# Kernel tuning notes

Hardware: AMD Instinct MI355X
Metric: run time of the kernel (lower is better)

## Reference

```python
import jax, jax.numpy as jnp
import numpy as np

NEG = -9e15  # mask value from original (-9000000000000000.0)

def setup_inputs() -> dict:
    key = jax.random.key(0)
    k1, k2, k3, k4 = jax.random.split(key, 4)
    N, nin, nout = 8192, 256, 128
    h = jax.random.normal(k1, (N, nin), dtype=jnp.float32)
    adj = jax.random.randint(k2, (N, N), 0, 2, dtype=jnp.int32)
    w = jax.random.normal(k3, (nin, nout), dtype=jnp.float32)
    v = jax.random.normal(k4, (2 * nout, 1), dtype=jnp.float32)
    return {"h": h, "adj": adj, "w": w, "v": v}

def reference(h, adj, w, v):
    nout = w.shape[1]
    hw = h @ w                      # [N, nout]
    hw1 = hw @ v[:nout]             # [N, 1]
    hw2 = hw @ v[nout:]             # [N, 1]
    eij = hw1 + hw2.T               # [N, N] additive outer-sum scores
    att = jnp.where(adj > 0, eij, jnp.float32(NEG))
    att = jax.nn.softmax(att, axis=1)
    return att @ hw                 # [N, nout]
```

## Files before the change

### kernel.cpp

```cpp
#include <hip/hip_runtime.h>
#include <math.h>

#define N_ROWS 8192
#define NIN    256
#define NOUT   128
#define CUTOFF 45.0f
#define TOPK   32
#define NBINS  256
#define RANGE  384.0f
#define MAXL   256

__device__ __forceinline__ float block_max_256(float v, float* red) {
#pragma unroll
    for (int off = 32; off > 0; off >>= 1)
        v = fmaxf(v, __shfl_down(v, off, 64));
    if ((threadIdx.x & 63) == 0) red[threadIdx.x >> 6] = v;
    __syncthreads();
    float r = fmaxf(fmaxf(red[0], red[1]), fmaxf(red[2], red[3]));
    __syncthreads();
    return r;
}

__global__ __launch_bounds__(256) void k_sw(const float* __restrict__ h,
                                            const float* __restrict__ w,
                                            const float* __restrict__ v,
                                            float* __restrict__ s) {
    __shared__ float wv[NIN];
    int tid = threadIdx.x;
    const float* wr = w + (size_t)tid * NOUT;
    const float* v2 = v + NOUT;
    float acc = 0.f;
#pragma unroll
    for (int n = 0; n < NOUT; n += 4) {
        float4 a = *(const float4*)(wr + n);
        float4 b = *(const float4*)(v2 + n);
        acc = fmaf(a.x, b.x, acc);
        acc = fmaf(a.y, b.y, acc);
        acc = fmaf(a.z, b.z, acc);
        acc = fmaf(a.w, b.w, acc);
    }
    wv[tid] = acc;
    __syncthreads();

    int wid  = tid >> 6;
    int lane = tid & 63;
    float4 wv4 = *(const float4*)(wv + lane * 4);
    int row0 = blockIdx.x * 8 + wid * 2;
#pragma unroll
    for (int r = 0; r < 2; ++r) {
        const float* hr = h + (size_t)(row0 + r) * NIN;
        float4 hv = *(const float4*)(hr + lane * 4);
        float a = hv.x * wv4.x;
        a = fmaf(hv.y, wv4.y, a);
        a = fmaf(hv.z, wv4.z, a);
        a = fmaf(hv.w, wv4.w, a);
#pragma unroll
        for (int off = 32; off > 0; off >>= 1)
            a += __shfl_down(a, off, 64);
        if (lane == 0) s[row0 + r] = a;
    }
}

__global__ __launch_bounds__(256) void k_top(const float* __restrict__ s_g,
                                             int* __restrict__ L,
                                             float* __restrict__ Ls,
                                             int* __restrict__ nL_p,
                                             float* __restrict__ T_p) {
    __shared__ float sd[N_ROWS];
    __shared__ float red[4];
    __shared__ int   hist[NBINS];
    __shared__ int   c;
    __shared__ float Tsh;
    int tid = threadIdx.x;
    hist[tid] = 0;
    float mloc = -INFINITY;
    for (int j = tid; j < N_ROWS; j += 256) {
        float v = s_g[j];
        sd[j] = v;
        mloc = fmaxf(mloc, v);
    }
    __syncthreads();
    float mstar = block_max_256(mloc, red);
    const float invw = (float)NBINS / RANGE;
    for (int j = tid; j < N_ROWS; j += 256) {
        int b = (int)((mstar - sd[j]) * invw);
        b = b < 0 ? 0 : (b > NBINS - 1 ? NBINS - 1 : b);
        atomicAdd(&hist[b], 1);
    }
    __syncthreads();
    if (tid == 0) {
        int cum = 0, B = NBINS - 1;
        for (int b = 0; b < NBINS; ++b) {
            cum += hist[b];
            if (cum >= TOPK) { B = b; break; }
        }
        Tsh = mstar - (float)(B + 1) * (RANGE / (float)NBINS) - CUTOFF;
        *T_p = Tsh;
        c = 0;
    }
    __syncthreads();
    float T = Tsh;
    for (int j = tid; j < N_ROWS; j += 256) {
        float v = sd[j];
        if (v >= T) {
            int p = atomicAdd(&c, 1);
            L[p]  = j;
            Ls[p] = v;
        }
    }
    __syncthreads();
    if (tid == 0) *nL_p = c;
}

__global__ __launch_bounds__(128) void k_hwL(const float* __restrict__ h,
                                             const float* __restrict__ w,
                                             const int* __restrict__ L,
                                             const int* __restrict__ nL_p,
                                             float* __restrict__ hwL2) {
    int nL = *nL_p;
    if (nL > MAXL) return;
    int nLp = (nL + 7) & ~7;
    int k = threadIdx.x;
    int sidx = ((k & 63) << 1) | (k >> 6);
    for (int t = blockIdx.x; t < nLp; t += gridDim.x) {
        float acc = 0.f;
        if (t < nL) {
            const float* hr = h + (size_t)L[t] * NIN;
#pragma unroll 4
            for (int n = 0; n < NIN; n += 4) {
                float4 hv = *(const float4*)(hr + n);
                acc = fmaf(hv.x, w[(size_t)(n + 0) * NOUT + k], acc);
                acc = fmaf(hv.y, w[(size_t)(n + 1) * NOUT + k], acc);
                acc = fmaf(hv.z, w[(size_t)(n + 2) * NOUT + k], acc);
                acc = fmaf(hv.w, w[(size_t)(n + 3) * NOUT + k], acc);
            }
        }
        hwL2[(size_t)t * NOUT + sidx] = acc;
    }
}

__global__ __launch_bounds__(256) void k_att6(const int* __restrict__ adj,
                                              const float* __restrict__ s_g,
                                              const float* __restrict__ h,
                                              const float* __restrict__ w,
                                              const float* __restrict__ hwL2,
                                              const int* __restrict__ L,
                                              const float* __restrict__ Ls,
                                              const int* __restrict__ nL_p,
                                              const float* __restrict__ T_p,
                                              float* __restrict__ out) {
    int wid  = threadIdx.x >> 6;
    int lane = threadIdx.x & 63;
    int i    = blockIdx.x * 4 + wid;
    int   nL = nL_p[0];
    float T  = T_p[0];
    const int* arow = adj + (size_t)i * N_ROWS;

    bool fast = (nL <= MAXL);
    float sv[4] = {-INFINITY, -INFINITY, -INFINITY, -INFINITY};
    float m = -INFINITY;

    if (fast) {
#pragma unroll
        for (int p = 0; p < 4; ++p) {
            int t = p * 64 + lane;
            if (t < nL) {
                int j = L[t];
                sv[p] = (arow[j] > 0) ? Ls[t] : -INFINITY;
            }
        }
        float mm = fmaxf(fmaxf(sv[0], sv[1]), fmaxf(sv[2], sv[3]));
#pragma unroll
        for (int off = 32; off > 0; off >>= 1)
            mm = fmaxf(mm, __shfl_down(mm, off, 64));
        m = __shfl(mm, 0, 64);
    }

    if (fast && (m - CUTOFF >= T)) {
        float pw[4];
        float dp = 0.f;
#pragma unroll
        for (int p = 0; p < 4; ++p) {
            pw[p] = __expf(sv[p] - m);
            dp += pw[p];
        }
#pragma unroll
        for (int off = 32; off > 0; off >>= 1)
            dp += __shfl_down(dp, off, 64);
        float den = __shfl(dp, 0, 64);

        float th = m - CUTOFF;
        float acc0 = 0.f, acc1 = 0.f;
#pragma unroll
        for (int p = 0; p < 4; ++p) {
            unsigned long long bm = __ballot(sv[p] >= th);
            while (bm) {
                int t0 = __ffsll((long long)bm) - 1;
                bm &= bm - 1;
                float pwt = __shfl(pw[p], t0, 64);
                const float* g = hwL2 + (size_t)(p * 64 + t0) * NOUT + (lane << 1);
                float2 gv = *(const float2*)g;
                acc0 = fmaf(pwt, gv.x, acc0);
                acc1 = fmaf(pwt, gv.y, acc1);
            }
        }
        out[(size_t)i * NOUT + lane]      = acc0 / den;
        out[(size_t)i * NOUT + 64 + lane] = acc1 / den;
        return;
    }

    float m2 = -INFINITY;
    for (int j0 = lane * 4; j0 < N_ROWS; j0 += 256) {
        int4   a  = *(const int4*)(arow + j0);
        float4 sx = *(const float4*)(s_g + j0);
        if (a.x > 0) m2 = fmaxf(m2, sx.x);
        if (a.y > 0) m2 = fmaxf(m2, sx.y);
        if (a.z > 0) m2 = fmaxf(m2, sx.z);
        if (a.w > 0) m2 = fmaxf(m2, sx.w);
    }
#pragma unroll
    for (int off = 32; off > 0; off >>= 1)
        m2 = fmaxf(m2, __shfl_down(m2, off, 64));
    m2 = __shfl(m2, 0, 64);

    if (m2 > -INFINITY) {
        float acc0 = 0.f, acc1 = 0.f, den = 0.f;
        for (int j = 0; j < N_ROWS; ++j) {
            if (arow[j] > 0) {
                float p = __expf(s_g[j] - m2);
                if (p > 0.f) {
                    den += p;
                    const float* hr = h + (size_t)j * NIN;
                    float d0 = 0.f, d1 = 0.f;
                    for (int nn = 0; nn < NIN; ++nn) {
                        float hv = hr[nn];
                        d0 = fmaf(hv, w[(size_t)nn * NOUT + lane], d0);
                        d1 = fmaf(hv, w[(size_t)nn * NOUT + 64 + lane], d1);
                    }
                    acc0 = fmaf(p, d0, acc0);
                    acc1 = fmaf(p, d1, acc1);
                }
            }
        }
        out[(size_t)i * NOUT + lane]      = acc0 / den;
        out[(size_t)i * NOUT + 64 + lane] = acc1 / den;
    } else {
        float cs[4] = {0.f, 0.f, 0.f, 0.f};
        for (int r = 0; r < N_ROWS; ++r) {
            const float* hr = h + (size_t)r * NIN;
#pragma unroll
            for (int q = 0; q < 4; ++q)
                cs[q] += hr[lane + q * 64];
        }
        float acc0 = 0.f, acc1 = 0.f;
        for (int nn = 0; nn < NIN; ++nn) {
            float csv = __shfl(cs[nn >> 6], nn & 63, 64);
            acc0 = fmaf(csv, w[(size_t)nn * NOUT + lane], acc0);
            acc1 = fmaf(csv, w[(size_t)nn * NOUT + 64 + lane], acc1);
        }
        out[(size_t)i * NOUT + lane]      = acc0 / (float)N_ROWS;
        out[(size_t)i * NOUT + 64 + lane] = acc1 / (float)N_ROWS;
    }
}

extern "C" void kernel_launch(void* const* d_in, const int* in_sizes, int n_in,
                              void* d_out, int out_size, void* d_ws, size_t ws_size,
                              hipStream_t stream) {
    const float* h   = (const float*)d_in[0];
    const int*   adj = (const int*)  d_in[1];
    const float* w   = (const float*)d_in[2];
    const float* v   = (const float*)d_in[3];
    float* out = (float*)d_out;

    char* ws = (char*)d_ws;
    float* hwL = (float*)(ws);
    size_t o   = (size_t)MAXL * NOUT * 4;
    float* s   = (float*)(ws + o);  o += (size_t)N_ROWS * 4;
    int*   L   = (int*)  (ws + o);  o += (size_t)N_ROWS * 4;
    float* Ls  = (float*)(ws + o);  o += (size_t)N_ROWS * 4;
    int*   nL  = (int*)  (ws + o);  o += 16;
    float* T   = (float*)(ws + o);

    k_sw  <<<N_ROWS / 8, 256, 0, stream>>>(h, w, v, s);
    k_top <<<1,          256, 0, stream>>>(s, L, Ls, nL, T);
    k_hwL <<<128,        128, 0, stream>>>(h, w, L, nL, hwL);
    k_att6<<<N_ROWS / 4, 256, 0, stream>>>(adj, s, h, w, hwL, L, Ls, nL, T, out);
}
```

Baseline: 375.1 us.

## Fuse candidate projection into top-k kernel and split slow fallback rows out

The hwL projection of candidate rows moves into the single-block top-k kernel, which removes one launch but computes the projections with only 256 threads. The slow fallback path leaves the attention kernel: rows that need it are queued with an atomic counter, and a separate k_fix kernel processes them. This frees the main attention kernel of heavy fallback code so it can use fewer registers and run at higher occupancy (launch_bounds 256,8). In exchange there is an extra launch, and the serial top-k block now does more work.

```diff
diff --git a/kernel.cpp b/kernel.cpp
--- a/kernel.cpp
+++ b/kernel.cpp
@@ -61,16 +61,21 @@
     }
 }
 
-__global__ __launch_bounds__(256) void k_top(const float* __restrict__ s_g,
-                                             int* __restrict__ L,
-                                             float* __restrict__ Ls,
-                                             int* __restrict__ nL_p,
-                                             float* __restrict__ T_p) {
+__global__ __launch_bounds__(256) void k_topw(const float* __restrict__ s_g,
+                                              const float* __restrict__ h,
+                                              const float* __restrict__ w,
+                                              int* __restrict__ L,
+                                              float* __restrict__ Ls,
+                                              int* __restrict__ nL_p,
+                                              float* __restrict__ T_p,
+                                              float* __restrict__ hwL2,
+                                              int* __restrict__ nU_p) {
     __shared__ float sd[N_ROWS];
     __shared__ float red[4];
     __shared__ int   hist[NBINS];
     __shared__ int   c;
     __shared__ float Tsh;
+    __shared__ int   Lsh[MAXL];
     int tid = threadIdx.x;
     hist[tid] = 0;
     float mloc = -INFINITY;
@@ -97,6 +102,7 @@
         Tsh = mstar - (float)(B + 1) * (RANGE / (float)NBINS) - CUTOFF;
         *T_p = Tsh;
         c = 0;
+        *nU_p = 0;
     }
     __syncthreads();
     float T = Tsh;
@@ -106,26 +112,21 @@
             int p = atomicAdd(&c, 1);
             L[p]  = j;
             Ls[p] = v;
-        }
-    }
-    __syncthreads();
-    if (tid == 0) *nL_p = c;
-}
-
-__global__ __launch_bounds__(128) void k_hwL(const float* __restrict__ h,
-                                             const float* __restrict__ w,
-                                             const int* __restrict__ L,
-                                             const int* __restrict__ nL_p,
-                                             float* __restrict__ hwL2) {
-    int nL = *nL_p;
+            if (p < MAXL) Lsh[p] = j;
+        }
+    }
+    __syncthreads();
+    int nL = c;
+    if (tid == 0) *nL_p = nL;
     if (nL > MAXL) return;
-    int nLp = (nL + 7) & ~7;
-    int k = threadIdx.x;
+
+    int nLp  = (nL + 7) & ~7;
+    int k    = tid & 127;
     int sidx = ((k & 63) << 1) | (k >> 6);
-    for (int t = blockIdx.x; t < nLp; t += gridDim.x) {
+    for (int t = tid >> 7; t < nLp; t += 2) {
         float acc = 0.f;
         if (t < nL) {
-            const float* hr = h + (size_t)L[t] * NIN;
+            const float* hr = h + (size_t)Lsh[t] * NIN;
 #pragma unroll 4
             for (int n = 0; n < NIN; n += 4) {
                 float4 hv = *(const float4*)(hr + n);
@@ -139,16 +140,15 @@
     }
 }
 
-__global__ __launch_bounds__(256) void k_att6(const int* __restrict__ adj,
-                                              const float* __restrict__ s_g,
-                                              const float* __restrict__ h,
-                                              const float* __restrict__ w,
-                                              const float* __restrict__ hwL2,
-                                              const int* __restrict__ L,
-                                              const float* __restrict__ Ls,
-                                              const int* __restrict__ nL_p,
-                                              const float* __restrict__ T_p,
-                                              float* __restrict__ out) {
+__global__ __launch_bounds__(256, 8) void k_att7(const int* __restrict__ adj,
+                                                 const float* __restrict__ hwL2,
+                                                 const int* __restrict__ L,
+                                                 const float* __restrict__ Ls,
+                                                 const int* __restrict__ nL_p,
+                                                 const float* __restrict__ T_p,
+                                                 float* __restrict__ out,
+                                                 int* __restrict__ UL,
+                                                 int* __restrict__ nU_p) {
     int wid  = threadIdx.x >> 6;
     int lane = threadIdx.x & 63;
     int i    = blockIdx.x * 4 + wid;
@@ -209,57 +209,78 @@
         return;
     }
 
-    float m2 = -INFINITY;
-    for (int j0 = lane * 4; j0 < N_ROWS; j0 += 256) {
-        int4   a  = *(const int4*)(arow + j0);
-        float4 sx = *(const float4*)(s_g + j0);
-        if (a.x > 0) m2 = fmaxf(m2, sx.x);
-        if (a.y > 0) m2 = fmaxf(m2, sx.y);
-        if (a.z > 0) m2 = fmaxf(m2, sx.z);
-        if (a.w > 0) m2 = fmaxf(m2, sx.w);
-    }
-#pragma unroll
-    for (int off = 32; off > 0; off >>= 1)
-        m2 = fmaxf(m2, __shfl_down(m2, off, 64));
-    m2 = __shfl(m2, 0, 64);
-
-    if (m2 > -INFINITY) {
-        float acc0 = 0.f, acc1 = 0.f, den = 0.f;
-        for (int j = 0; j < N_ROWS; ++j) {
-            if (arow[j] > 0) {
-                float p = __expf(s_g[j] - m2);
-                if (p > 0.f) {
-                    den += p;
-                    const float* hr = h + (size_t)j * NIN;
-                    float d0 = 0.f, d1 = 0.f;
-                    for (int nn = 0; nn < NIN; ++nn) {
-                        float hv = hr[nn];
-                        d0 = fmaf(hv, w[(size_t)nn * NOUT + lane], d0);
-                        d1 = fmaf(hv, w[(size_t)nn * NOUT + 64 + lane], d1);
+    if (lane == 0) {
+        int p = atomicAdd(nU_p, 1);
+        UL[p] = i;
+    }
+}
+
+__global__ __launch_bounds__(256) void k_fix(const int* __restrict__ adj,
+                                             const float* __restrict__ s_g,
+                                             const float* __restrict__ h,
+                                             const float* __restrict__ w,
+                                             const int* __restrict__ UL,
+                                             const int* __restrict__ nU_p,
+                                             float* __restrict__ out) {
+    int nU = nU_p[0];
+    if (nU == 0) return;
+    int wid  = threadIdx.x >> 6;
+    int lane = threadIdx.x & 63;
+    for (int u = blockIdx.x * 4 + wid; u < nU; u += gridDim.x * 4) {
+        int i = UL[u];
+        const int* arow = adj + (size_t)i * N_ROWS;
+        float m2 = -INFINITY;
+        for (int j0 = lane * 4; j0 < N_ROWS; j0 += 256) {
+            int4   a  = *(const int4*)(arow + j0);
+            float4 sx = *(const float4*)(s_g + j0);
+            if (a.x > 0) m2 = fmaxf(m2, sx.x);
+            if (a.y > 0) m2 = fmaxf(m2, sx.y);
+            if (a.z > 0) m2 = fmaxf(m2, sx.z);
+            if (a.w > 0) m2 = fmaxf(m2, sx.w);
+        }
+#pragma unroll
+        for (int off = 32; off > 0; off >>= 1)
+            m2 = fmaxf(m2, __shfl_down(m2, off, 64));
+        m2 = __shfl(m2, 0, 64);
+
+        if (m2 > -INFINITY) {
+            float acc0 = 0.f, acc1 = 0.f, den = 0.f;
+            for (int j = 0; j < N_ROWS; ++j) {
+                if (arow[j] > 0) {
+                    float p = __expf(s_g[j] - m2);
+                    if (p > 0.f) {
+                        den += p;
+                        const float* hr = h + (size_t)j * NIN;
+                        float d0 = 0.f, d1 = 0.f;
+                        for (int nn = 0; nn < NIN; ++nn) {
+                            float hv = hr[nn];
+                            d0 = fmaf(hv, w[(size_t)nn * NOUT + lane], d0);
+                            d1 = fmaf(hv, w[(size_t)nn * NOUT + 64 + lane], d1);
+                        }
+                        acc0 = fmaf(p, d0, acc0);
+                        acc1 = fmaf(p, d1, acc1);
                     }
-                    acc0 = fmaf(p, d0, acc0);
-                    acc1 = fmaf(p, d1, acc1);
                 }
             }
-        }
-        out[(size_t)i * NOUT + lane]      = acc0 / den;
-        out[(size_t)i * NOUT + 64 + lane] = acc1 / den;
-    } else {
-        float cs[4] = {0.f, 0.f, 0.f, 0.f};
-        for (int r = 0; r < N_ROWS; ++r) {
-            const float* hr = h + (size_t)r * NIN;
-#pragma unroll
-            for (int q = 0; q < 4; ++q)
-                cs[q] += hr[lane + q * 64];
-        }
-        float acc0 = 0.f, acc1 = 0.f;
-        for (int nn = 0; nn < NIN; ++nn) {
-            float csv = __shfl(cs[nn >> 6], nn & 63, 64);
-            acc0 = fmaf(csv, w[(size_t)nn * NOUT + lane], acc0);
-            acc1 = fmaf(csv, w[(size_t)nn * NOUT + 64 + lane], acc1);
-        }
-        out[(size_t)i * NOUT + lane]      = acc0 / (float)N_ROWS;
-        out[(size_t)i * NOUT + 64 + lane] = acc1 / (float)N_ROWS;
+            out[(size_t)i * NOUT + lane]      = acc0 / den;
+            out[(size_t)i * NOUT + 64 + lane] = acc1 / den;
+        } else {
+            float cs[4] = {0.f, 0.f, 0.f, 0.f};
+            for (int r = 0; r < N_ROWS; ++r) {
+                const float* hr = h + (size_t)r * NIN;
+#pragma unroll
+                for (int q = 0; q < 4; ++q)
+                    cs[q] += hr[lane + q * 64];
+            }
+            float acc0 = 0.f, acc1 = 0.f;
+            for (int nn = 0; nn < NIN; ++nn) {
+                float csv = __shfl(cs[nn >> 6], nn & 63, 64);
+                acc0 = fmaf(csv, w[(size_t)nn * NOUT + lane], acc0);
+                acc1 = fmaf(csv, w[(size_t)nn * NOUT + 64 + lane], acc1);
+            }
+            out[(size_t)i * NOUT + lane]      = acc0 / (float)N_ROWS;
+            out[(size_t)i * NOUT + 64 + lane] = acc1 / (float)N_ROWS;
+        }
     }
 }
 
@@ -278,11 +299,13 @@
     float* s   = (float*)(ws + o);  o += (size_t)N_ROWS * 4;
     int*   L   = (int*)  (ws + o);  o += (size_t)N_ROWS * 4;
     float* Ls  = (float*)(ws + o);  o += (size_t)N_ROWS * 4;
+    int*   UL  = (int*)  (ws + o);  o += (size_t)N_ROWS * 4;
     int*   nL  = (int*)  (ws + o);  o += 16;
-    float* T   = (float*)(ws + o);
+    float* T   = (float*)(ws + o);  o += 16;
+    int*   nU  = (int*)  (ws + o);
 
     k_sw  <<<N_ROWS / 8, 256, 0, stream>>>(h, w, v, s);
-    k_top <<<1,          256, 0, stream>>>(s, L, Ls, nL, T);
-    k_hwL <<<128,        128, 0, stream>>>(h, w, L, nL, hwL);
-    k_att6<<<N_ROWS / 4, 256, 0, stream>>>(adj, s, h, w, hwL, L, Ls, nL, T, out);
-}
+    k_topw<<<1,          256, 0, stream>>>(s, h, w, L, Ls, nL, T, hwL, nU);
+    k_att7<<<N_ROWS / 4, 256, 0, stream>>>(adj, hwL, L, Ls, nL, T, out, UL, nU);
+    k_fix <<<2048,       256, 0, stream>>>(adj, s, h, w, UL, nU, out);
+}
```

After: 553.9 us. 47.7% more time.
